# Performance work log

Hardware: AMD Instinct MI355X
Metric: run time of the kernel (lower is better)

Reference implementation:

```python
import jax, jax.numpy as jnp
import numpy as np

KK = 9  # 3x3 kernel points
PAD = 1
EPS = 1e-5


def _conv2d(x, w, b):
    # x: [B,C,H,W], w: [O,I,3,3]
    y = jax.lax.conv_general_dilated(
        x, w, window_strides=(1, 1), padding=((PAD, PAD), (PAD, PAD)),
        dimension_numbers=("NCHW", "OIHW", "NCHW"))
    return y + b[None, :, None, None]


def _bilinear_sample_one(img, py, px):
    # img: [C,H,W]; py, px: [KK,H,W] fractional sample coords
    C, H, W = img.shape
    y0 = jnp.floor(py).astype(jnp.int32)
    x0 = jnp.floor(px).astype(jnp.int32)
    wy = py - y0
    wx = px - x0

    def g(yi, xi):
        ok = ((yi >= 0) & (yi < H) & (xi >= 0) & (xi < W)).astype(img.dtype)
        v = img[:, jnp.clip(yi, 0, H - 1), jnp.clip(xi, 0, W - 1)]  # [C,KK,H,W]
        return v * ok[None]

    v00 = g(y0, x0)
    v01 = g(y0, x0 + 1)
    v10 = g(y0 + 1, x0)
    v11 = g(y0 + 1, x0 + 1)
    return (v00 * (1 - wy) * (1 - wx) + v01 * (1 - wy) * wx
            + v10 * wy * (1 - wx) + v11 * wy * wx)  # [C,KK,H,W]


def setup_inputs() -> dict:
    key = jax.random.key(0)
    ks = jax.random.split(key, 8)
    B, C, H, W = 8, 256, 96, 96
    O = 256
    x = jax.random.normal(ks[0], (B, C, H, W), dtype=jnp.float32)
    # modulated DCNv2 offset/mask conv: 3*KK output channels
    w_off = jax.random.normal(ks[1], (3 * KK, C, 3, 3), dtype=jnp.float32) * 0.01
    b_off = jnp.zeros((3 * KK,), dtype=jnp.float32)
    w_dcn = jax.random.normal(ks[2], (O, C, 3, 3), dtype=jnp.float32) * (1.0 / np.sqrt(C * KK))
    b_dcn = jnp.zeros((O,), dtype=jnp.float32)
    gamma = jnp.ones((O,), dtype=jnp.float32)
    beta = jnp.zeros((O,), dtype=jnp.float32)
    running_mean = jax.random.normal(ks[3], (O,), dtype=jnp.float32) * 0.1
    running_var = jax.random.uniform(ks[4], (O,), dtype=jnp.float32, minval=0.5, maxval=1.5)
    return {"x": x, "w_off": w_off, "b_off": b_off, "w_dcn": w_dcn,
            "b_dcn": b_dcn, "gamma": gamma, "beta": beta,
            "running_mean": running_mean, "running_var": running_var}


def reference(x, w_off, b_off, w_dcn, b_dcn, gamma, beta, running_mean, running_var):
    B, C, H, W = x.shape
    O = w_dcn.shape[0]
    # offsets + modulation masks
    om = _conv2d(x, w_off, b_off)                  # [B, 3*KK, H, W]
    offset = om[:, :2 * KK]
    mask = jax.nn.sigmoid(om[:, 2 * KK:])          # [B, KK, H, W]
    off_y = offset[:, 0::2]                        # [B, KK, H, W]
    off_x = offset[:, 1::2]

    ky, kx = jnp.meshgrid(jnp.arange(3), jnp.arange(3), indexing="ij")
    ky = ky.reshape(KK).astype(x.dtype)
    kx = kx.reshape(KK).astype(x.dtype)
    hh = jnp.arange(H, dtype=x.dtype)
    ww = jnp.arange(W, dtype=x.dtype)
    # fractional sampling coordinates per output pixel per kernel point
    py = off_y + hh[None, None, :, None] + ky[None, :, None, None] - PAD
    px = off_x + ww[None, None, None, :] + kx[None, :, None, None] - PAD

    sampled = jax.vmap(_bilinear_sample_one)(x, py, px)  # [B,C,KK,H,W]
    sampled = sampled * mask[:, None]
    out = jnp.einsum("bckhw,ock->bohw", sampled, w_dcn.reshape(O, C, KK))
    out = out + b_dcn[None, :, None, None]
    # BatchNorm (inference, running stats) + ReLU
    inv = jax.lax.rsqrt(running_var + EPS)
    out = (out - running_mean[None, :, None, None]) * (gamma * inv)[None, :, None, None]
    out = out + beta[None, :, None, None]
    return jax.nn.relu(out)
```

## Files before the change

kernel.cpp:

```cpp
#include <hip/hip_runtime.h>
#include <hip/hip_bf16.h>
#include <cstdint>
#include <cstddef>

#define H 96
#define W 96
#define HW 9216
#define C 256
#define B 8
#define O 256
#define KK 9
#define EPS 1e-5f

typedef __attribute__((ext_vector_type(8))) short short8;
typedef __attribute__((ext_vector_type(4))) float float4v;
typedef __attribute__((ext_vector_type(2))) float float2v;
typedef unsigned short ushort_t;
typedef unsigned int uint_t;

__global__ __launch_bounds__(256) void transpose_x_k(
    const float* __restrict__ x, ushort_t* __restrict__ xt)
{
    __shared__ float tile[64][65];
    int t = threadIdx.x;
    int p0 = blockIdx.x * 64;
    int c0 = blockIdx.y * 64;
    int b  = blockIdx.z;
    {
        int tx = t & 63, ty = t >> 6;
        const float* xb = x + ((size_t)b * C + c0 + ty) * HW + p0 + tx;
#pragma unroll
        for (int i = 0; i < 64; i += 4)
            tile[ty + i][tx] = xb[(size_t)i * HW];
    }
    __syncthreads();
    {
        int tc = t & 31, tp = t >> 5;
        ushort_t* xtb = xt + ((size_t)b * HW + p0) * C + c0;
#pragma unroll
        for (int i = 0; i < 64; i += 8) {
            int p = tp + i;
            float a  = tile[2 * tc][p];
            float bb = tile[2 * tc + 1][p];
            __hip_bfloat162 h2 = __float22bfloat162_rn(make_float2(a, bb));
            uint_t u;
            __builtin_memcpy(&u, &h2, 4);
            *reinterpret_cast<uint_t*>(&xtb[(size_t)p * C + 2 * tc]) = u;
        }
    }
}

__global__ __launch_bounds__(256) void prep_b_k(
    const float* __restrict__ wd, ushort_t* __restrict__ bp)
{
    int idx = blockIdx.x * 256 + threadIdx.x;
    int kk = idx / (O * C);
    int r = idx - kk * O * C;
    int o = r >> 8, c = r & 255;
    float v = wd[((size_t)o * C + c) * KK + kk];
    __hip_bfloat16 hh = __float2bfloat16(v);
    ushort_t u;
    __builtin_memcpy(&u, &hh, 2);
    bp[idx] = u;
}

__global__ __launch_bounds__(256) void prep_bo_k(
    const float* __restrict__ wo, ushort_t* __restrict__ bo)
{
    int idx = blockIdx.x * 256 + threadIdx.x;
    int n = idx / (KK * C);
    int r = idx - n * KK * C;
    int kk = r >> 8, c = r & 255;
    float v = (n < 27) ? wo[((size_t)n * C + c) * KK + kk] : 0.0f;
    __hip_bfloat16 hh = __float2bfloat16(v);
    ushort_t u;
    __builtin_memcpy(&u, &hh, 2);
    bo[idx] = u;
}

__global__ __launch_bounds__(256) void offset_mfma_k(
    const ushort_t* __restrict__ xt, const ushort_t* __restrict__ bo,
    const float* __restrict__ b_off, float* __restrict__ om)
{
    int t = threadIdx.x;
    int wv = t >> 6, l = t & 63;
    int ln = l & 15, lq = l >> 4;
    int d = blockIdx.x;
    int lb = (d & 7) * 72 + (d >> 3);
    int p0 = lb * 128;
    int b = p0 / HW;
    int rem0w = p0 - b * HW + wv * 32;
    const ushort_t* xtb = xt + (size_t)b * HW * C;

    int hh0[2], ww0[2];
#pragma unroll
    for (int mt = 0; mt < 2; ++mt) {
        int rem = rem0w + mt * 16 + ln;
        hh0[mt] = rem / W;
        ww0[mt] = rem - hh0[mt] * W;
    }

    float4v acc[2][2];
#pragma unroll
    for (int i = 0; i < 2; ++i)
#pragma unroll
        for (int j = 0; j < 2; ++j) acc[i][j] = (float4v){0.f, 0.f, 0.f, 0.f};

#pragma unroll
    for (int kk = 0; kk < KK; ++kk) {
        int dy = kk / 3 - 1, dx = kk % 3 - 1;
        const ushort_t* ap[2];
        uint_t msk[2];
#pragma unroll
        for (int mt = 0; mt < 2; ++mt) {
            int hh = hh0[mt] + dy, ww = ww0[mt] + dx;
            bool ok = (hh >= 0) & (hh < H) & (ww >= 0) & (ww < W);
            msk[mt] = ok ? 0xffffffffu : 0u;
            int hc = min(max(hh, 0), H - 1);
            int wc = min(max(ww, 0), W - 1);
            ap[mt] = xtb + (size_t)(hc * W + wc) * C + lq * 8;
        }
        const ushort_t* bp0 = bo + ((size_t)(0 * 16 + ln) * KK + kk) * C + lq * 8;
        const ushort_t* bp1 = bo + ((size_t)(1 * 16 + ln) * KK + kk) * C + lq * 8;
#pragma unroll
        for (int cc = 0; cc < 8; ++cc) {
            int c0 = cc * 32;
            short8 af[2];
#pragma unroll
            for (int mt = 0; mt < 2; ++mt) {
                uint4 u = *(const uint4*)(ap[mt] + c0);
                u.x &= msk[mt]; u.y &= msk[mt]; u.z &= msk[mt]; u.w &= msk[mt];
                __builtin_memcpy(&af[mt], &u, 16);
            }
            short8 bf0 = *(const short8*)(bp0 + c0);
            short8 bf1 = *(const short8*)(bp1 + c0);
#pragma unroll
            for (int mt = 0; mt < 2; ++mt) {
                acc[mt][0] = __builtin_amdgcn_mfma_f32_16x16x32_bf16(af[mt], bf0, acc[mt][0], 0, 0, 0);
                acc[mt][1] = __builtin_amdgcn_mfma_f32_16x16x32_bf16(af[mt], bf1, acc[mt][1], 0, 0, 0);
            }
        }
    }

    float* omb = om + (size_t)b * 27 * HW + rem0w;
#pragma unroll
    for (int nt = 0; nt < 2; ++nt) {
        int oc = nt * 16 + ln;
        if (oc < 27) {
            float bv = b_off[oc];
            float* po = omb + (size_t)oc * HW + lq * 4;
#pragma unroll
            for (int mt = 0; mt < 2; ++mt) {
                float4 v;
                v.x = acc[mt][nt].x + bv;
                v.y = acc[mt][nt].y + bv;
                v.z = acc[mt][nt].z + bv;
                v.w = acc[mt][nt].w + bv;
                *(float4*)(po + mt * 16) = v;
            }
        }
    }
}

__device__ __forceinline__ float2v up2(uint_t u) {
    float2v r;
    r.x = __uint_as_float(u << 16);
    r.y = __uint_as_float(u & 0xffff0000u);
    return r;
}

__device__ __forceinline__ uint_t packbf2(float a, float b) {
    __hip_bfloat162 h2 = __float22bfloat162_rn(make_float2(a, b));
    uint_t u;
    __builtin_memcpy(&u, &h2, 4);
    return u;
}

__global__ __launch_bounds__(256) void dcn_main_k(
    const ushort_t* __restrict__ xt, const float* __restrict__ om,
    const ushort_t* __restrict__ bp, const float* __restrict__ b_dcn,
    const float* __restrict__ gamma, const float* __restrict__ beta,
    const float* __restrict__ rmean, const float* __restrict__ rvar,
    float* __restrict__ out)
{
    __shared__ uint4    s_rec0[64 * KK];
    __shared__ float2   s_rec1[64 * KK];
    __shared__ ushort_t s_a[2][8][64][32];

    int t = threadIdx.x;
    int d = blockIdx.x;
    int lb = (d & 7) * 144 + (d >> 3);
    int p0 = lb * 64;
    int b = p0 / HW;
    int rem0 = p0 - b * HW;

    for (int v = t; v < 64 * KK; v += 256) {
        int m = v & 63;
        int k = v >> 6;
        int rem = rem0 + m;
        int h = rem / W;
        int w = rem - h * W;
        const float* omb = om + (size_t)b * 27 * HW + rem;
        float offy = omb[(size_t)(2 * k) * HW];
        float offx = omb[(size_t)(2 * k + 1) * HW];
        float z    = omb[(size_t)(18 + k) * HW];
        float mval = 1.0f / (1.0f + __expf(-z));
        float py = (float)(h + k / 3 - 1) + offy;
        float px = (float)(w + k % 3 - 1) + offx;
        float fy = floorf(py), fx = floorf(px);
        int y0 = (int)fy, x0 = (int)fx;
        float wy = py - fy, wx = px - fx;
        float row0f = (1.0f - wy) * mval * ((y0 >= 0 && y0 < H) ? 1.0f : 0.0f);
        float row1f = wy * mval * ((y0 >= -1 && y0 < H - 1) ? 1.0f : 0.0f);
        int xsel = min(max(x0, 0), W - 2);
        float wxa = (x0 >= 0 && x0 < W) ? (1.0f - wx) : 0.0f;
        float wxb = (x0 >= -1 && x0 < W - 1) ? wx : 0.0f;
        int cx0 = min(max(x0, 0), W - 1);
        int cx1 = min(max(x0 + 1, 0), W - 1);
        float wA = ((cx0 == xsel) ? wxa : 0.0f) + ((cx1 == xsel) ? wxb : 0.0f);
        float wB = ((cx0 == xsel + 1) ? wxa : 0.0f) + ((cx1 == xsel + 1) ? wxb : 0.0f);
        int yc0 = min(max(y0, 0), H - 1);
        int yc1 = min(max(y0 + 1, 0), H - 1);
        uint4 r0;
        r0.x = (uint_t)((yc0 * W + xsel) * C);
        r0.y = (uint_t)((yc1 * W + xsel) * C);
        r0.z = __float_as_uint(row0f * wA);
        r0.w = __float_as_uint(row0f * wB);
        s_rec0[v] = r0;
        s_rec1[v] = make_float2(row1f * wA, row1f * wB);
    }

    float4v acc[4][4];
#pragma unroll
    for (int i = 0; i < 4; ++i)
#pragma unroll
        for (int j = 0; j < 4; ++j)
            acc[i][j] = (float4v){0.f, 0.f, 0.f, 0.f};

    const ushort_t* xtb = xt + (size_t)b * HW * C;
    int wv = t >> 6;
    int l  = t & 63;
    int ln = l & 15;
    int lq = l >> 4;
    int sm = t >> 2;
    int sc = (t & 3) * 8;

    __syncthreads();

#define COMBINE(L0_, L1_, L2_, L3_, W_, dst_) do {                          \
        uint4 pk_;                                                          \
        float2v r0_ = up2((L0_).x) * (W_)[0] + up2((L1_).x) * (W_)[1]       \
                    + up2((L2_).x) * (W_)[2] + up2((L3_).x) * (W_)[3];      \
        float2v r1_ = up2((L0_).y) * (W_)[0] + up2((L1_).y) * (W_)[1]       \
                    + up2((L2_).y) * (W_)[2] + up2((L3_).y) * (W_)[3];      \
        float2v r2_ = up2((L0_).z) * (W_)[0] + up2((L1_).z) * (W_)[1]       \
                    + up2((L2_).z) * (W_)[2] + up2((L3_).z) * (W_)[3];      \
        float2v r3_ = up2((L0_).w) * (W_)[0] + up2((L1_).w) * (W_)[1]       \
                    + up2((L2_).w) * (W_)[2] + up2((L3_).w) * (W_)[3];      \
        pk_.x = packbf2(r0_.x, r0_.y);                                      \
        pk_.y = packbf2(r1_.x, r1_.y);                                      \
        pk_.z = packbf2(r2_.x, r2_.y);                                      \
        pk_.w = packbf2(r3_.x, r3_.y);                                      \
        *(uint4*)(dst_) = pk_;                                              \
    } while (0)

    {
        uint4 r0 = s_rec0[sm];
        float2 r1 = s_rec1[sm];
        const ushort_t* a0 = xtb + r0.x + sc;
        const ushort_t* a1 = xtb + r0.y + sc;
        float Wt[4] = {__uint_as_float(r0.z), __uint_as_float(r0.w), r1.x, r1.y};
#pragma unroll
        for (int ci = 0; ci < 8; ++ci) {
            uint4 L0 = *(const uint4*)(a0 + ci * 32);
            uint4 L1 = *(const uint4*)(a0 + ci * 32 + C);
            uint4 L2 = *(const uint4*)(a1 + ci * 32);
            uint4 L3 = *(const uint4*)(a1 + ci * 32 + C);
            COMBINE(L0, L1, L2, L3, Wt, &s_a[0][ci][sm][sc]);
        }
    }
    __syncthreads();

    for (int kk = 0; kk < KK; ++kk) {
        int rb = kk & 1;
        int wb = rb ^ 1;
        bool more = (kk < KK - 1);

        const ushort_t* a0n = xtb;
        const ushort_t* a1n = xtb;
        float Wn[4] = {0.f, 0.f, 0.f, 0.f};
        if (more) {
            uint4 r0 = s_rec0[(kk + 1) * 64 + sm];
            float2 r1 = s_rec1[(kk + 1) * 64 + sm];
            a0n = xtb + r0.x + sc;
            a1n = xtb + r0.y + sc;
            Wn[0] = __uint_as_float(r0.z); Wn[1] = __uint_as_float(r0.w);
            Wn[2] = r1.x; Wn[3] = r1.y;
        }

        const ushort_t* bpk = bp + ((size_t)kk * O + wv * 64 + ln) * C + lq * 8;
        short8 bfr[4], bfrN[4];
#pragma unroll
        for (int nt = 0; nt < 4; ++nt)
            bfr[nt] = *(const short8*)(bpk + (size_t)nt * 16 * C);

#pragma unroll
        for (int ci = 0; ci < 8; ++ci) {
            uint4 L0, L1, L2, L3;
            if (more) {
                L0 = *(const uint4*)(a0n + ci * 32);
                L1 = *(const uint4*)(a0n + ci * 32 + C);
                L2 = *(const uint4*)(a1n + ci * 32);
                L3 = *(const uint4*)(a1n + ci * 32 + C);
            }
            if (ci < 7) {
#pragma unroll
                for (int nt = 0; nt < 4; ++nt)
                    bfrN[nt] = *(const short8*)(bpk + (size_t)nt * 16 * C + (ci + 1) * 32);
            }
            short8 af[4];
#pragma unroll
            for (int mt = 0; mt < 4; ++mt)
                af[mt] = *(const short8*)&s_a[rb][ci][mt * 16 + ln][lq * 8];
#pragma unroll
            for (int mt = 0; mt < 4; ++mt)
#pragma unroll
                for (int nt = 0; nt < 4; ++nt)
                    acc[mt][nt] = __builtin_amdgcn_mfma_f32_16x16x32_bf16(
                        af[mt], bfr[nt], acc[mt][nt], 0, 0, 0);
            if (more)
                COMBINE(L0, L1, L2, L3, Wn, &s_a[wb][ci][sm][sc]);
#pragma unroll
            for (int nt = 0; nt < 4; ++nt)
                bfr[nt] = bfrN[nt];
        }
        __syncthreads();
    }
#undef COMBINE

#pragma unroll
    for (int nt = 0; nt < 4; ++nt) {
        int o = wv * 64 + nt * 16 + ln;
        float scale = gamma[o] * rsqrtf(rvar[o] + EPS);
        float shift = (b_dcn[o] - rmean[o]) * scale + beta[o];
        float* po = out + ((size_t)b * O + o) * HW + rem0 + lq * 4;
#pragma unroll
        for (int mt = 0; mt < 4; ++mt) {
            float4 vv;
            vv.x = fmaxf(acc[mt][nt].x * scale + shift, 0.0f);
            vv.y = fmaxf(acc[mt][nt].y * scale + shift, 0.0f);
            vv.z = fmaxf(acc[mt][nt].z * scale + shift, 0.0f);
            vv.w = fmaxf(acc[mt][nt].w * scale + shift, 0.0f);
            *(float4*)(po + mt * 16) = vv;
        }
    }
}

extern "C" void kernel_launch(void* const* d_in, const int* in_sizes, int n_in,
                              void* d_out, int out_size, void* d_ws, size_t ws_size,
                              hipStream_t stream) {
    const float* x     = (const float*)d_in[0];
    const float* w_off = (const float*)d_in[1];
    const float* b_off = (const float*)d_in[2];
    const float* w_dcn = (const float*)d_in[3];
    const float* b_dcn = (const float*)d_in[4];
    const float* gamma = (const float*)d_in[5];
    const float* beta  = (const float*)d_in[6];
    const float* rmean = (const float*)d_in[7];
    const float* rvar  = (const float*)d_in[8];
    float* out = (float*)d_out;

    float*    om  = (float*)d_ws;
    ushort_t* bpw = (ushort_t*)(om + (size_t)B * 27 * HW);
    ushort_t* bow = bpw + (size_t)KK * O * C;
    ushort_t* xtw = bow + (size_t)32 * KK * C;

    hipLaunchKernelGGL(transpose_x_k, dim3(144, 4, 8), dim3(256), 0, stream,
                       x, xtw);
    hipLaunchKernelGGL(prep_b_k, dim3(2304), dim3(256), 0, stream,
                       w_dcn, bpw);
    hipLaunchKernelGGL(prep_bo_k, dim3(288), dim3(256), 0, stream,
                       w_off, bow);
    hipLaunchKernelGGL(offset_mfma_k, dim3(73728 / 128), dim3(256), 0, stream,
                       xtw, bow, b_off, om);
    hipLaunchKernelGGL(dcn_main_k, dim3(73728 / 64), dim3(256), 0, stream,
                       xtw, om, bpw, b_dcn, gamma, beta, rmean, rvar, out);
}
```

Measured before the change: 457.3 us.

## Halve LDS staging per phase and compress sampling records to raise occupancy

The main DCN kernel now splits each kernel tap into two half-channel phases, so the double-buffered bf16 A tile shrinks from 8 to 4 channel chunks per buffer. The per-pixel sampling records are packed into a uint3 holding 16-bit pixel indices and fp16 row and column weights, which cuts LDS further. Launch bounds request 4 blocks per SM. The goal is more resident blocks to hide gather latency, at the cost of twice as many barriers per tile and fp16 rounding of the bilinear weights.

```diff
diff --git a/kernel.cpp b/kernel.cpp
--- a/kernel.cpp
+++ b/kernel.cpp
@@ -1,5 +1,6 @@
 #include <hip/hip_runtime.h>
 #include <hip/hip_bf16.h>
+#include <hip/hip_fp16.h>
 #include <cstdint>
 #include <cstddef>
 
@@ -176,16 +177,15 @@
     return u;
 }
 
-__global__ __launch_bounds__(256) void dcn_main_k(
+__global__ __launch_bounds__(256, 4) void dcn_main_k(
     const ushort_t* __restrict__ xt, const float* __restrict__ om,
     const ushort_t* __restrict__ bp, const float* __restrict__ b_dcn,
     const float* __restrict__ gamma, const float* __restrict__ beta,
     const float* __restrict__ rmean, const float* __restrict__ rvar,
     float* __restrict__ out)
 {
-    __shared__ uint4    s_rec0[64 * KK];
-    __shared__ float2   s_rec1[64 * KK];
-    __shared__ ushort_t s_a[2][8][64][32];
+    __shared__ uint3    s_rec[64 * KK];
+    __shared__ ushort_t s_a[2][4][64][32];
 
     int t = threadIdx.x;
     int d = blockIdx.x;
@@ -221,13 +221,13 @@
         float wB = ((cx0 == xsel + 1) ? wxa : 0.0f) + ((cx1 == xsel + 1) ? wxb : 0.0f);
         int yc0 = min(max(y0, 0), H - 1);
         int yc1 = min(max(y0 + 1, 0), H - 1);
-        uint4 r0;
-        r0.x = (uint_t)((yc0 * W + xsel) * C);
-        r0.y = (uint_t)((yc1 * W + xsel) * C);
-        r0.z = __float_as_uint(row0f * wA);
-        r0.w = __float_as_uint(row0f * wB);
-        s_rec0[v] = r0;
-        s_rec1[v] = make_float2(row1f * wA, row1f * wB);
+        uint3 rr;
+        rr.x = (uint_t)(yc0 * W + xsel) | ((uint_t)(yc1 * W + xsel) << 16);
+        __half2 h01 = __floats2half2_rn(row0f, row1f);
+        __half2 hAB = __floats2half2_rn(wA, wB);
+        __builtin_memcpy(&rr.y, &h01, 4);
+        __builtin_memcpy(&rr.z, &hAB, 4);
+        s_rec[v] = rr;
     }
 
     float4v acc[4][4];
@@ -246,6 +246,20 @@
     int sc = (t & 3) * 8;
 
     __syncthreads();
+
+#define DECREC(rr_, cb_, a0_, a1_, Wt_) do {                                \
+        int px0_ = (rr_).x & 0xffff;                                        \
+        int px1_ = (rr_).x >> 16;                                           \
+        (a0_) = xtb + (size_t)px0_ * C + (cb_) + sc;                        \
+        (a1_) = xtb + (size_t)px1_ * C + (cb_) + sc;                        \
+        __half2 h01_, hAB_;                                                 \
+        __builtin_memcpy(&h01_, &(rr_).y, 4);                               \
+        __builtin_memcpy(&hAB_, &(rr_).z, 4);                               \
+        float r0_ = __low2float(h01_), r1_ = __high2float(h01_);            \
+        float wa_ = __low2float(hAB_), wb_ = __high2float(hAB_);            \
+        (Wt_)[0] = r0_ * wa_; (Wt_)[1] = r0_ * wb_;                         \
+        (Wt_)[2] = r1_ * wa_; (Wt_)[3] = r1_ * wb_;                         \
+    } while (0)
 
 #define COMBINE(L0_, L1_, L2_, L3_, W_, dst_) do {                          \
         uint4 pk_;                                                          \
@@ -265,13 +279,12 @@
     } while (0)
 
     {
-        uint4 r0 = s_rec0[sm];
-        float2 r1 = s_rec1[sm];
-        const ushort_t* a0 = xtb + r0.x + sc;
-        const ushort_t* a1 = xtb + r0.y + sc;
-        float Wt[4] = {__uint_as_float(r0.z), __uint_as_float(r0.w), r1.x, r1.y};
-#pragma unroll
-        for (int ci = 0; ci < 8; ++ci) {
+        uint3 rr = s_rec[sm];
+        const ushort_t *a0, *a1;
+        float Wt[4];
+        DECREC(rr, 0, a0, a1, Wt);
+#pragma unroll
+        for (int ci = 0; ci < 4; ++ci) {
             uint4 L0 = *(const uint4*)(a0 + ci * 32);
             uint4 L1 = *(const uint4*)(a0 + ci * 32 + C);
             uint4 L2 = *(const uint4*)(a1 + ci * 32);
@@ -281,31 +294,29 @@
     }
     __syncthreads();
 
-    for (int kk = 0; kk < KK; ++kk) {
-        int rb = kk & 1;
+    for (int ph = 0; ph < 2 * KK; ++ph) {
+        int rb = ph & 1;
         int wb = rb ^ 1;
-        bool more = (kk < KK - 1);
+        bool more = (ph < 2 * KK - 1);
+        int tap = ph >> 1, hf = ph & 1;
 
         const ushort_t* a0n = xtb;
         const ushort_t* a1n = xtb;
         float Wn[4] = {0.f, 0.f, 0.f, 0.f};
         if (more) {
-            uint4 r0 = s_rec0[(kk + 1) * 64 + sm];
-            float2 r1 = s_rec1[(kk + 1) * 64 + sm];
-            a0n = xtb + r0.x + sc;
-            a1n = xtb + r0.y + sc;
-            Wn[0] = __uint_as_float(r0.z); Wn[1] = __uint_as_float(r0.w);
-            Wn[2] = r1.x; Wn[3] = r1.y;
-        }
-
-        const ushort_t* bpk = bp + ((size_t)kk * O + wv * 64 + ln) * C + lq * 8;
+            int np = ph + 1;
+            uint3 rr = s_rec[(np >> 1) * 64 + sm];
+            DECREC(rr, (np & 1) * 128, a0n, a1n, Wn);
+        }
+
+        const ushort_t* bpk = bp + ((size_t)tap * O + wv * 64 + ln) * C + hf * 128 + lq * 8;
         short8 bfr[4], bfrN[4];
 #pragma unroll
         for (int nt = 0; nt < 4; ++nt)
             bfr[nt] = *(const short8*)(bpk + (size_t)nt * 16 * C);
 
 #pragma unroll
-        for (int ci = 0; ci < 8; ++ci) {
+        for (int ci = 0; ci < 4; ++ci) {
             uint4 L0, L1, L2, L3;
             if (more) {
                 L0 = *(const uint4*)(a0n + ci * 32);
@@ -313,7 +324,7 @@
                 L2 = *(const uint4*)(a1n + ci * 32);
                 L3 = *(const uint4*)(a1n + ci * 32 + C);
             }
-            if (ci < 7) {
+            if (ci < 3) {
 #pragma unroll
                 for (int nt = 0; nt < 4; ++nt)
                     bfrN[nt] = *(const short8*)(bpk + (size_t)nt * 16 * C + (ci + 1) * 32);
@@ -337,6 +348,7 @@
         __syncthreads();
     }
 #undef COMBINE
+#undef DECREC
 
 #pragma unroll
     for (int nt = 0; nt < 4; ++nt) {
```

Measured after the change: 684.5 us. +49.7%, slower.
